# Optimization experiments

Hardware: AMD Instinct MI355X
Metric: run time of the kernel (lower is better)

The kernel has to match this reference:

```python
import jax, jax.numpy as jnp
import numpy as np

B, N, DIM = 2, 2048, 1024
HEADS, DIM_HEAD = 16, 64
ALIBI_HEADS = 8
NUM_MEM_KV = 4
SCALE = DIM_HEAD ** -0.5


def alibi_slopes(n):
    # standard ALiBi geometric slopes for power-of-2 head counts
    start = 2.0 ** (-8.0 / n)
    return jnp.array([start ** (k + 1) for k in range(n)], dtype=jnp.float32)


def alibi_bias(i, j, heads, total_heads):
    # symmetric ALiBi: bias = -|k_pos - q_pos| * slope; unbiased heads padded with zeros at front
    range_q = jnp.arange(j - i, j)          # query absolute positions (offset by mem kv)
    range_k = jnp.arange(j)
    rel = -jnp.abs(range_k[None, :] - range_q[:, None]).astype(jnp.float32)  # [i, j]
    slopes = alibi_slopes(heads)
    bias = slopes[:, None, None] * rel[None]                                  # [heads, i, j]
    pad = jnp.zeros((total_heads - heads, i, j), dtype=bias.dtype)
    return jnp.concatenate([pad, bias], axis=0)                               # [total_heads, i, j]


def setup_inputs() -> dict:
    key = jax.random.key(0)
    ks = jax.random.split(key, 7)
    w = lambda k, s: jax.random.normal(k, s, jnp.float32) * 0.02
    return {
        "x": jax.random.normal(ks[0], (B, N, DIM), jnp.float32),
        "mask": jnp.ones((B, N), dtype=bool),
        "Wq": w(ks[1], (DIM, HEADS * DIM_HEAD)),
        "Wk": w(ks[2], (DIM, HEADS * DIM_HEAD)),
        "Wv": w(ks[3], (DIM, HEADS * DIM_HEAD)),
        "Wo": w(ks[4], (HEADS * DIM_HEAD, DIM)),
        "mem_k": jax.random.normal(ks[5], (HEADS, NUM_MEM_KV, DIM_HEAD), jnp.float32),
        "mem_v": jax.random.normal(ks[6], (HEADS, NUM_MEM_KV, DIM_HEAD), jnp.float32),
    }


def reference(x, mask, Wq, Wk, Wv, Wo, mem_k, mem_v):
    b, n, _ = x.shape
    h, d, m = HEADS, DIM_HEAD, NUM_MEM_KV
    # QKV projections (Linear, no bias)
    q = (x @ Wq).reshape(b, n, h, d).transpose(0, 2, 1, 3)  # [b,h,n,d]
    k = (x @ Wk).reshape(b, n, h, d).transpose(0, 2, 1, 3)
    v = (x @ Wv).reshape(b, n, h, d).transpose(0, 2, 1, 3)
    # prepend learned memory key/values
    k = jnp.concatenate([jnp.broadcast_to(mem_k[None], (b, h, m, d)), k], axis=2)
    v = jnp.concatenate([jnp.broadcast_to(mem_v[None], (b, h, m, d)), v], axis=2)
    i, j = n, n + m
    # input mask padded with True over memory positions
    input_mask = jnp.concatenate([jnp.ones((b, m), dtype=bool), mask], axis=1)  # [b,j]
    # causal mask: key kj attendable by query qi iff kj - (j - i) <= qi (mem keys always visible)
    qpos = jnp.arange(i)[:, None]
    kpos = jnp.arange(j)[None, :]
    causal_allow = (kpos - (j - i)) <= qpos                                      # [i,j]
    allow = input_mask[:, None, None, :] & causal_allow[None, None]              # [b,1,i,j]
    bias = alibi_bias(i, j, ALIBI_HEADS, h)                                      # [h,i,j]
    scores = jnp.einsum('bhid,bhjd->bhij', q, k) * SCALE + bias[None]
    scores = jnp.where(allow, scores, jnp.finfo(scores.dtype).min)
    attn = jax.nn.softmax(scores, axis=-1)
    out = jnp.einsum('bhij,bhjd->bhid', attn, v)
    out = out.transpose(0, 2, 1, 3).reshape(b, n, h * d) @ Wo
    return out * mask[..., None].astype(out.dtype)
```

## Files before the change

### kernel.cpp

```cpp
#include <hip/hip_runtime.h>

typedef __bf16 bf16x8 __attribute__((ext_vector_type(8)));
typedef float f32x4 __attribute__((ext_vector_type(4)));
typedef unsigned short us8 __attribute__((ext_vector_type(8)));
typedef unsigned short ushort_t;
typedef unsigned int uint_t;

constexpr int BATCH = 2;
constexpr int SEQ   = 2048;
constexpr int DIM   = 1024;
constexpr int HEADS = 16;
constexpr int DH    = 64;
constexpr int NKV   = 4;
constexpr int KROWS = 2080;
constexpr int KVSTR = 133120;
constexpr float QSCALE = 0.18033688011112042f;

__device__ inline ushort_t f2bf(float f) {
  uint_t u = __builtin_bit_cast(uint_t, f);
  u += 0x7FFFu + ((u >> 16) & 1u);
  return (ushort_t)(u >> 16);
}

__device__ inline uint_t cvtpk(float a, float b) {
  uint_t r;
  asm("v_cvt_pk_bf16_f32 %0, %1, %2" : "=v"(r) : "v"(a), "v"(b));
  return r;
}

__device__ inline float ex2(float x) { return __builtin_amdgcn_exp2f(x); }

__device__ inline bf16x8 mk8(uint_t a, uint_t b, uint_t c, uint_t d) {
  union { uint_t u[4]; bf16x8 v; } x;
  x.u[0] = a; x.u[1] = b; x.u[2] = c; x.u[3] = d;
  return x.v;
}

__device__ inline size_t swz(int row, int k) {
  return ((size_t)(row >> 7) << 17) +
         (size_t)(((k >> 3) << 7) + (row & 127)) * 8 + (k & 7);
}

__device__ inline int koff(int j, int d) {
  return ((j >> 4) << 10) + ((d >> 3) << 7) + ((j & 15) << 3) + (d & 7);
}
__device__ inline int voff(int j, int d) {
  int w = j & 31;
  int kap = ((w & 12) << 1) | (w & 3) | ((w >> 4) << 2);
  return ((j >> 5) << 11) + ((kap >> 3) << 9) + (d << 3) + (kap & 7);
}

__device__ inline void g2l16(const ushort_t* g, ushort_t* l) {
  __builtin_amdgcn_global_load_lds(
      (const __attribute__((address_space(1))) void*)g,
      (__attribute__((address_space(3))) void*)l, 16, 0, 0);
}

__global__ __launch_bounds__(256) void prep_kernel(
    const float* __restrict__ x,
    const float* __restrict__ W0, const float* __restrict__ W1,
    const float* __restrict__ W2, const float* __restrict__ W3,
    const float* __restrict__ memk, const float* __restrict__ memv,
    ushort_t* __restrict__ xb,
    ushort_t* __restrict__ T0, ushort_t* __restrict__ T1,
    ushort_t* __restrict__ T2, ushort_t* __restrict__ T3,
    ushort_t* __restrict__ Vt, ushort_t* __restrict__ Ka)
{
  __shared__ float tile[32][33];
  int bid = blockIdx.x, t = threadIdx.x;
  if (bid < 2048) {
    int idx = bid * 256 + t;
    const float4* s = (const float4*)x;
    float4 a = s[idx * 2], bq = s[idx * 2 + 1];
    us8 o;
    o[0] = f2bf(a.x);  o[1] = f2bf(a.y);  o[2] = f2bf(a.z);  o[3] = f2bf(a.w);
    o[4] = f2bf(bq.x); o[5] = f2bf(bq.y); o[6] = f2bf(bq.z); o[7] = f2bf(bq.w);
    int e = idx * 8, row = e >> 10, k = e & 1023;
    *(us8*)&xb[swz(row, k)] = o;
  } else if (bid < 6144) {
    int tb = bid - 2048, z = tb >> 10, r2 = tb & 1023;
    int bx = r2 & 31, by = r2 >> 5;
    const float* W = (z == 0) ? W0 : (z == 1) ? W1 : (z == 2) ? W2 : W3;
    ushort_t* T = (z == 0) ? T0 : (z == 1) ? T1 : (z == 2) ? T2 : T3;
    float sc = (z == 0) ? QSCALE : 1.0f;
    int tx = t & 31, ty = t >> 5;
    int kb = bx * 32, nb = by * 32;
    for (int y = ty; y < 32; y += 8)
      tile[y][tx] = W[(size_t)(kb + y) * 1024 + nb + tx];
    __syncthreads();
    for (int y = ty; y < 32; y += 8)
      T[swz(nb + y, kb + tx)] = f2bf(tile[tx][y] * sc);
  } else {
    int idx = (bid - 6144) * 256 + t;
    if (idx < 8192) {
      int j = idx & 3, d = (idx >> 2) & 63, h = (idx >> 8) & 15, b = idx >> 12;
      Vt[(size_t)(b * 16 + h) * KVSTR + voff(j, d)] =
          f2bf(memv[((size_t)h * NKV + j) * DH + d]);
    } else if (idx < 16384) {
      int k2 = idx - 8192;
      int d = k2 & 63, j = (k2 >> 6) & 3, h = (k2 >> 8) & 15, b = k2 >> 12;
      Ka[(size_t)(b * 16 + h) * KVSTR + koff(j, d)] =
          f2bf(memk[((size_t)h * NKV + j) * DH + d]);
    }
  }
}

__global__ __launch_bounds__(256, 6) void gemm_bt(
    const ushort_t* __restrict__ A,
    const ushort_t* __restrict__ Wt0, const ushort_t* __restrict__ Wt1,
    const ushort_t* __restrict__ Wt2,
    ushort_t* __restrict__ C0, ushort_t* __restrict__ Ka,
    ushort_t* __restrict__ Vt)
{
  __shared__ ushort_t As[8192];
  __shared__ ushort_t Bs[4096];
  int bid = blockIdx.x;
  int xcd = bid & 7, g = bid >> 3;
  int z = g >> 6, rem = g & 63;
  int my = (xcd >> 1) * 8 + (rem >> 3);
  int nx = (xcd & 1) * 8 + (rem & 7);
  const ushort_t* Wt = (z == 1) ? Wt1 : (z == 2) ? Wt2 : Wt0;
  int t = threadIdx.x;
  int lane = t & 63, wave = t >> 6;
  int col = lane & 15, quad = lane >> 4;
  int m0 = my * 128, n0 = nx * 64;
  int moff = wave * 32;
  int nhalf = nx & 1;

  const ushort_t* Abase = A  + ((size_t)(m0 >> 7) << 17);
  const ushort_t* Bbase = Wt + ((size_t)(nx >> 1) << 17);
  int so = wave * 2048 + lane * 8;

  f32x4 acc[2][4] = {};

  for (int k0 = 0; k0 < DIM; k0 += 64) {
    __syncthreads();
    const ushort_t* Ak = Abase + ((size_t)k0 << 7);
    const ushort_t* Bk = Bbase + ((size_t)k0 << 7);
#pragma unroll
    for (int c2 = 0; c2 < 4; c2++)
      g2l16(Ak + so + c2 * 512, &As[so + c2 * 512]);
#pragma unroll
    for (int c2 = 0; c2 < 2; c2++) {
      int ko = wave * 2 + c2;
      g2l16(Bk + ko * 1024 + nhalf * 512 + lane * 8, &Bs[ko * 512 + lane * 8]);
    }
    __syncthreads();
#pragma unroll
    for (int kc = 0; kc < 2; kc++) {
      bf16x8 af[2], bfr[4];
#pragma unroll
      for (int mi = 0; mi < 2; mi++)
        af[mi] = *(const bf16x8*)&As[(kc * 4 + quad) * 1024 + (moff + mi * 16 + col) * 8];
#pragma unroll
      for (int ni = 0; ni < 4; ni++)
        bfr[ni] = *(const bf16x8*)&Bs[(kc * 4 + quad) * 512 + (ni * 16 + col) * 8];
#pragma unroll
      for (int mi = 0; mi < 2; mi++)
#pragma unroll
        for (int ni = 0; ni < 4; ni++)
          acc[mi][ni] = __builtin_amdgcn_mfma_f32_16x16x32_bf16(
              af[mi], bfr[ni], acc[mi][ni], 0, 0, 0);
    }
  }

  if (z == 0) {
#pragma unroll
    for (int mi = 0; mi < 2; mi++) {
      int row0 = m0 + moff + mi * 16 + quad * 4;
#pragma unroll
      for (int ni = 0; ni < 4; ni++) {
        int cn = n0 + ni * 16 + col;
#pragma unroll
        for (int r = 0; r < 4; r++)
          C0[swz(row0 + r, cn)] = f2bf(acc[mi][ni][r]);
      }
    }
  } else if (z == 1) {
#pragma unroll
    for (int mi = 0; mi < 2; mi++) {
      int gi = m0 + moff + mi * 16 + quad * 4;
      int bq = gi >> 11, i = gi & 2047;
#pragma unroll
      for (int ni = 0; ni < 4; ni++) {
        int feat = n0 + ni * 16 + col;
        int hh = feat >> 6, dd = feat & 63;
        size_t base = (size_t)(bq * 16 + hh) * KVSTR;
#pragma unroll
        for (int r = 0; r < 4; r++)
          Ka[base + koff(i + r + NKV, dd)] = f2bf(acc[mi][ni][r]);
      }
    }
  } else {
#pragma unroll
    for (int mi = 0; mi < 2; mi++) {
      int gi = m0 + moff + mi * 16 + quad * 4;
      int bq = gi >> 11, i = gi & 2047;
#pragma unroll
      for (int ni = 0; ni < 4; ni++) {
        int feat = n0 + ni * 16 + col;
        int hh = feat >> 6, dd = feat & 63;
        size_t vb = (size_t)(bq * 16 + hh) * KVSTR;
#pragma unroll
        for (int r = 0; r < 4; r++)
          Vt[vb + voff(i + r + NKV, dd)] = f2bf(acc[mi][ni][r]);
      }
    }
  }
}

__global__ __launch_bounds__(256, 4) void gemm_out64(
    const ushort_t* __restrict__ A, const ushort_t* __restrict__ Wt,
    float* __restrict__ Cf)
{
  __shared__ ushort_t As[4096];
  __shared__ ushort_t Bs[4096];
  int bid = blockIdx.x;
  int xcd = bid & 7, g = bid >> 3;
  int my = xcd * 8 + (g >> 4);
  int nx = g & 15;
  int t = threadIdx.x;
  int lane = t & 63, wave = t >> 6;
  int col = lane & 15, quad = lane >> 4;
  int m0 = my * 64, n0 = nx * 64;
  int mhalf = my & 1;
  int nhalf = nx & 1;

  const ushort_t* Abase = A  + ((size_t)(my >> 1) << 17);
  const ushort_t* Bbase = Wt + ((size_t)(nx >> 1) << 17);

  f32x4 acc[4] = {};

  for (int k0 = 0; k0 < DIM; k0 += 64) {
    __syncthreads();
    const ushort_t* Ak = Abase + ((size_t)k0 << 7);
    const ushort_t* Bk = Bbase + ((size_t)k0 << 7);
#pragma unroll
    for (int c2 = 0; c2 < 2; c2++) {
      int ko = wave * 2 + c2;
      g2l16(Ak + ko * 1024 + mhalf * 512 + lane * 8, &As[ko * 512 + lane * 8]);
      g2l16(Bk + ko * 1024 + nhalf * 512 + lane * 8, &Bs[ko * 512 + lane * 8]);
    }
    __syncthreads();
#pragma unroll
    for (int kc = 0; kc < 2; kc++) {
      bf16x8 af, bfr[4];
      af = *(const bf16x8*)&As[(kc * 4 + quad) * 512 + (wave * 16 + col) * 8];
#pragma unroll
      for (int ni = 0; ni < 4; ni++)
        bfr[ni] = *(const bf16x8*)&Bs[(kc * 4 + quad) * 512 + (ni * 16 + col) * 8];
#pragma unroll
      for (int ni = 0; ni < 4; ni++)
        acc[ni] = __builtin_amdgcn_mfma_f32_16x16x32_bf16(
            af, bfr[ni], acc[ni], 0, 0, 0);
    }
  }

  int row0 = m0 + wave * 16 + quad * 4;
#pragma unroll
  for (int ni = 0; ni < 4; ni++) {
    int cn = n0 + ni * 16 + col;
#pragma unroll
    for (int r = 0; r < 4; r++)
      Cf[(size_t)(row0 + r) * DIM + cn] = acc[ni][r];
  }
}

#define SUBITER(jbX, jpref, K0, K1, K2, K3, V0, V1, V2, V3)                   \
  {                                                                           \
    f32x4 s0a = {}, s1a = {}, s0b = {}, s1b = {};                             \
    __builtin_amdgcn_s_setprio(1);                                            \
    s0a = __builtin_amdgcn_mfma_f32_16x16x32_bf16(K0, qa0, s0a, 0, 0, 0);     \
    s0a = __builtin_amdgcn_mfma_f32_16x16x32_bf16(K1, qa1, s0a, 0, 0, 0);     \
    s1a = __builtin_amdgcn_mfma_f32_16x16x32_bf16(K2, qa0, s1a, 0, 0, 0);     \
    s1a = __builtin_amdgcn_mfma_f32_16x16x32_bf16(K3, qa1, s1a, 0, 0, 0);     \
    s0b = __builtin_amdgcn_mfma_f32_16x16x32_bf16(K0, qb0, s0b, 0, 0, 0);     \
    s0b = __builtin_amdgcn_mfma_f32_16x16x32_bf16(K1, qb1, s0b, 0, 0, 0);     \
    s1b = __builtin_amdgcn_mfma_f32_16x16x32_bf16(K2, qb0, s1b, 0, 0, 0);     \
    s1b = __builtin_amdgcn_mfma_f32_16x16x32_bf16(K3, qb1, s1b, 0, 0, 0);     \
    __builtin_amdgcn_s_setprio(0);                                            \
    int jc = (jpref) > 2048 ? 2048 : (jpref);                                 \
    int aK = jc * 64 + kOff;                                                  \
    K0 = *(const bf16x8*)&Kbh[aK];                                            \
    K1 = *(const bf16x8*)&Kbh[aK + 512];                                      \
    K2 = *(const bf16x8*)&Kbh[aK + 1024];                                     \
    K3 = *(const bf16x8*)&Kbh[aK + 1536];                                     \
    float fD0 = (float)((jbX) + quad * 4 - i0 - col - NKV);                   \
    bf16x8 pa, pb;                                                            \
    {                                                                         \
      f32x4 e0, e1;                                                           \
      if ((jbX) <= i0 - 27) {                                                 \
        _Pragma("unroll")                                                     \
        for (int r = 0; r < 4; r++) {                                         \
          e0[r] = ex2(fmaf(slope2, fD0 + (float)r, s0a[r]));                  \
          e1[r] = ex2(fmaf(slope2, fD0 + 16.0f + (float)r, s1a[r]));          \
        }                                                                     \
      } else {                                                                \
        _Pragma("unroll")                                                     \
        for (int r = 0; r < 4; r++) {                                         \
          float f0 = fD0 + (float)r, f1 = fD0 + 16.0f + (float)r;             \
          float w0 = fmaf(slope2, f0, s0a[r]);                                \
          float w1 = fmaf(slope2, f1, s1a[r]);                                \
          w0 = (f0 <= 0.0f) ? w0 : -1e30f;                                    \
          w1 = (f1 <= 0.0f) ? w1 : -1e30f;                                    \
          e0[r] = ex2(w0); e1[r] = ex2(w1);                                   \
        }                                                                     \
      }                                                                       \
      pa = mk8(cvtpk(e0[0], e0[1]), cvtpk(e0[2], e0[3]),                      \
               cvtpk(e1[0], e1[1]), cvtpk(e1[2], e1[3]));                     \
    }                                                                         \
    {                                                                         \
      float fDb = fD0 - 16.0f;                                                \
      f32x4 e0, e1;                                                           \
      if ((jbX) <= i0 - 11) {                                                 \
        _Pragma("unroll")                                                     \
        for (int r = 0; r < 4; r++) {                                         \
          e0[r] = ex2(fmaf(slope2, fDb + (float)r, s0b[r]));                  \
          e1[r] = ex2(fmaf(slope2, fDb + 16.0f + (float)r, s1b[r]));          \
        }                                                                     \
      } else {                                                                \
        _Pragma("unroll")                                                     \
        for (int r = 0; r < 4; r++) {                                         \
          float f0 = fDb + (float)r, f1 = fDb + 16.0f + (float)r;             \
          float w0 = fmaf(slope2, f0, s0b[r]);                                \
          float w1 = fmaf(slope2, f1, s1b[r]);                                \
          w0 = (f0 <= 0.0f) ? w0 : -1e30f;                                    \
          w1 = (f1 <= 0.0f) ? w1 : -1e30f;                                    \
          e0[r] = ex2(w0); e1[r] = ex2(w1);                                   \
        }                                                                     \
      }                                                                       \
      pb = mk8(cvtpk(e0[0], e0[1]), cvtpk(e0[2], e0[3]),                      \
               cvtpk(e1[0], e1[1]), cvtpk(e1[2], e1[3]));                     \
    }                                                                         \
    __builtin_amdgcn_s_setprio(1);                                            \
    o0a = __builtin_amdgcn_mfma_f32_16x16x32_bf16(pa, V0, o0a, 0, 0, 0);      \
    o1a = __builtin_amdgcn_mfma_f32_16x16x32_bf16(pa, V1, o1a, 0, 0, 0);      \
    o2a = __builtin_amdgcn_mfma_f32_16x16x32_bf16(pa, V2, o2a, 0, 0, 0);      \
    o3a = __builtin_amdgcn_mfma_f32_16x16x32_bf16(pa, V3, o3a, 0, 0, 0);      \
    ola = __builtin_amdgcn_mfma_f32_16x16x32_bf16(pa, ones, ola, 0, 0, 0);    \
    o0b = __builtin_amdgcn_mfma_f32_16x16x32_bf16(pb, V0, o0b, 0, 0, 0);      \
    o1b = __builtin_amdgcn_mfma_f32_16x16x32_bf16(pb, V1, o1b, 0, 0, 0);      \
    o2b = __builtin_amdgcn_mfma_f32_16x16x32_bf16(pb, V2, o2b, 0, 0, 0);      \
    o3b = __builtin_amdgcn_mfma_f32_16x16x32_bf16(pb, V3, o3b, 0, 0, 0);      \
    olb = __builtin_amdgcn_mfma_f32_16x16x32_bf16(pb, ones, olb, 0, 0, 0);    \
    __builtin_amdgcn_s_setprio(0);                                            \
    int aV = jc * 64 + vOff;                                                  \
    V0 = *(const bf16x8*)&Vbh[aV];                                            \
    V1 = *(const bf16x8*)&Vbh[aV + 128];                                      \
    V2 = *(const bf16x8*)&Vbh[aV + 256];                                      \
    V3 = *(const bf16x8*)&Vbh[aV + 384];                                      \
  }

__global__ __launch_bounds__(256) void attn_kernel(
    const ushort_t* __restrict__ Q, const ushort_t* __restrict__ Ka,
    const ushort_t* __restrict__ Vt, ushort_t* __restrict__ AO)
{
  __shared__ __align__(16) float Cmb[2][10][64][4];
  int t = threadIdx.x, lane = t & 63, wave = t >> 6;
  int col = lane & 15, quad = lane >> 4;
  int bid = blockIdx.x;
  int xcd = bid & 7, slot = bid >> 3;
  int bh = xcd + 8 * (slot >> 4);
  int b = bh >> 4, h = bh & 15;
  int u = slot & 15;
  int pi = u * 2 + (wave >> 1);
  int h2 = wave & 1;
  int p2 = wave >> 1;
  float slope2 = (h < 8) ? 0.0f : exp2f(-(float)(h - 7)) * 1.4426950408889634f;

  const ushort_t* Kbh = Ka + (size_t)bh * KVSTR;
  const ushort_t* Vbh = Vt + (size_t)bh * KVSTR;

  us8 ones_u = {0x3F80, 0x3F80, 0x3F80, 0x3F80, 0x3F80, 0x3F80, 0x3F80, 0x3F80};
  bf16x8 ones = __builtin_bit_cast(bf16x8, ones_u);

  int kOff = quad * 128 + col * 8;
  int vOff = quad * 512 + col * 8;

  for (int hv = 0; hv < 2; hv++) {
    int s = hv ? 63 - pi : pi;
    int i0 = s * 32;
    int jend = ((i0 + 67) >> 5) << 5;

    bf16x8 qa0 = *(const bf16x8*)&Q[swz(b * SEQ + i0 + col, h * DH + quad * 8)];
    bf16x8 qa1 = *(const bf16x8*)&Q[swz(b * SEQ + i0 + col, h * DH + 32 + quad * 8)];
    bf16x8 qb0 = *(const bf16x8*)&Q[swz(b * SEQ + i0 + 16 + col, h * DH + quad * 8)];
    bf16x8 qb1 = *(const bf16x8*)&Q[swz(b * SEQ + i0 + 16 + col, h * DH + 32 + quad * 8)];

    f32x4 o0a = {}, o1a = {}, o2a = {}, o3a = {}, ola = {};
    f32x4 o0b = {}, o1b = {}, o2b = {}, o3b = {}, olb = {};

    bf16x8 ka0, ka1, ka2, ka3, va0, va1, va2, va3;
    bf16x8 kb0, kb1, kb2, kb3, vb0, vb1, vb2, vb3;
    int jb0 = h2 * 32;
    {
      int aK = jb0 * 64 + kOff, aV = jb0 * 64 + vOff;
      ka0 = *(const bf16x8*)&Kbh[aK];
      ka1 = *(const bf16x8*)&Kbh[aK + 512];
      ka2 = *(const bf16x8*)&Kbh[aK + 1024];
      ka3 = *(const bf16x8*)&Kbh[aK + 1536];
      va0 = *(const bf16x8*)&Vbh[aV];
      va1 = *(const bf16x8*)&Vbh[aV + 128];
      va2 = *(const bf16x8*)&Vbh[aV + 256];
      va3 = *(const bf16x8*)&Vbh[aV + 384];
      int j1 = jb0 + 64;
      int bK = j1 * 64 + kOff, bV = j1 * 64 + vOff;
      kb0 = *(const bf16x8*)&Kbh[bK];
      kb1 = *(const bf16x8*)&Kbh[bK + 512];
      kb2 = *(const bf16x8*)&Kbh[bK + 1024];
      kb3 = *(const bf16x8*)&Kbh[bK + 1536];
      vb0 = *(const bf16x8*)&Vbh[bV];
      vb1 = *(const bf16x8*)&Vbh[bV + 128];
      vb2 = *(const bf16x8*)&Vbh[bV + 256];
      vb3 = *(const bf16x8*)&Vbh[bV + 384];
    }

    int ntrip = (jend - jb0 + 127) >> 7;
    int jb = jb0;
#pragma unroll 1
    for (int tr = 0; tr < ntrip; tr++, jb += 128) {
      SUBITER(jb, jb + 128, ka0, ka1, ka2, ka3, va0, va1, va2, va3);
      SUBITER(jb + 64, jb + 192, kb0, kb1, kb2, kb3, vb0, vb1, vb2, vb3);
    }

    if (h2 == 1) {
      *(f32x4*)&Cmb[p2][0][lane][0] = o0a;
      *(f32x4*)&Cmb[p2][1][lane][0] = o1a;
      *(f32x4*)&Cmb[p2][2][lane][0] = o2a;
      *(f32x4*)&Cmb[p2][3][lane][0] = o3a;
      *(f32x4*)&Cmb[p2][4][lane][0] = ola;
      *(f32x4*)&Cmb[p2][5][lane][0] = o0b;
      *(f32x4*)&Cmb[p2][6][lane][0] = o1b;
      *(f32x4*)&Cmb[p2][7][lane][0] = o2b;
      *(f32x4*)&Cmb[p2][8][lane][0] = o3b;
      *(f32x4*)&Cmb[p2][9][lane][0] = olb;
    }
    __syncthreads();
    if (h2 == 0) {
      o0a += *(const f32x4*)&Cmb[p2][0][lane][0];
      o1a += *(const f32x4*)&Cmb[p2][1][lane][0];
      o2a += *(const f32x4*)&Cmb[p2][2][lane][0];
      o3a += *(const f32x4*)&Cmb[p2][3][lane][0];
      ola += *(const f32x4*)&Cmb[p2][4][lane][0];
      o0b += *(const f32x4*)&Cmb[p2][5][lane][0];
      o1b += *(const f32x4*)&Cmb[p2][6][lane][0];
      o2b += *(const f32x4*)&Cmb[p2][7][lane][0];
      o3b += *(const f32x4*)&Cmb[p2][8][lane][0];
      olb += *(const f32x4*)&Cmb[p2][9][lane][0];
#pragma unroll
      for (int r = 0; r < 4; r++) {
        float linv = __builtin_amdgcn_rcpf(ola[r]);
        int row = b * SEQ + i0 + quad * 4 + r;
        AO[swz(row, h * DH + col)]      = f2bf(o0a[r] * linv);
        AO[swz(row, h * DH + 16 + col)] = f2bf(o1a[r] * linv);
        AO[swz(row, h * DH + 32 + col)] = f2bf(o2a[r] * linv);
        AO[swz(row, h * DH + 48 + col)] = f2bf(o3a[r] * linv);
      }
#pragma unroll
      for (int r = 0; r < 4; r++) {
        float linv = __builtin_amdgcn_rcpf(olb[r]);
        int row = b * SEQ + i0 + 16 + quad * 4 + r;
        AO[swz(row, h * DH + col)]      = f2bf(o0b[r] * linv);
        AO[swz(row, h * DH + 16 + col)] = f2bf(o1b[r] * linv);
        AO[swz(row, h * DH + 32 + col)] = f2bf(o2b[r] * linv);
        AO[swz(row, h * DH + 48 + col)] = f2bf(o3b[r] * linv);
      }
    }
    __syncthreads();
  }
}
#undef SUBITER

extern "C" void kernel_launch(void* const* d_in, const int* in_sizes, int n_in,
                              void* d_out, int out_size, void* d_ws, size_t ws_size,
                              hipStream_t stream)
{
  const float* x    = (const float*)d_in[0];
  const float* Wq   = (const float*)d_in[2];
  const float* Wk   = (const float*)d_in[3];
  const float* Wv   = (const float*)d_in[4];
  const float* Wo   = (const float*)d_in[5];
  const float* memk = (const float*)d_in[6];
  const float* memv = (const float*)d_in[7];
  float* out = (float*)d_out;

  char* ws = (char*)d_ws;
  size_t off = 0;
  auto alloc = [&](size_t bytes) {
    char* p = ws + off;
    off += (bytes + 255) & ~(size_t)255;
    return p;
  };
  ushort_t* WqT = (ushort_t*)alloc((size_t)1024 * 1024 * 2);
  ushort_t* WkT = (ushort_t*)alloc((size_t)1024 * 1024 * 2);
  ushort_t* WvT = (ushort_t*)alloc((size_t)1024 * 1024 * 2);
  ushort_t* WoT = (ushort_t*)alloc((size_t)1024 * 1024 * 2);
  ushort_t* xb  = (ushort_t*)alloc((size_t)4096 * 1024 * 2);
  ushort_t* Qb  = (ushort_t*)alloc((size_t)4096 * 1024 * 2);
  ushort_t* Ka  = (ushort_t*)alloc((size_t)32 * KVSTR * 2);
  ushort_t* Vt  = (ushort_t*)alloc((size_t)32 * KVSTR * 2);
  ushort_t* AO  = xb;

  prep_kernel<<<dim3(6208), dim3(256), 0, stream>>>(
      x, Wq, Wk, Wv, Wo, memk, memv, xb, WqT, WkT, WvT, WoT, Vt, Ka);
  gemm_bt<<<dim3(1536), dim3(256), 0, stream>>>(xb, WqT, WkT, WvT, Qb, Ka, Vt);
  attn_kernel<<<dim3(512), dim3(256), 0, stream>>>(Qb, Ka, Vt, AO);
  gemm_out64<<<dim3(1024), dim3(256), 0, stream>>>(AO, WoT, out);
}
```

Measured before the change: 169.0 us.

## Fuse Q/K/V projection GEMMs into one block sharing the A tile

Each block now computes the Q, K and V output tiles for the same 128x64 region, loading the x tile once and three weight tiles per k-step. This replaces three separate blocks per tile, cutting redundant A-tile global loads and LDS fills to a third. Blocks grow to 512 threads with each wave owning 16 rows across three accumulators, so the grid shrinks from 1536 to 512 blocks. That may reduce occupancy and latency hiding, and it raises LDS use per block.

```diff
diff --git a/kernel.cpp b/kernel.cpp
--- a/kernel.cpp
+++ b/kernel.cpp
@@ -105,7 +105,7 @@
   }
 }
 
-__global__ __launch_bounds__(256, 6) void gemm_bt(
+__global__ __launch_bounds__(512) void gemm_bt(
     const ushort_t* __restrict__ A,
     const ushort_t* __restrict__ Wt0, const ushort_t* __restrict__ Wt1,
     const ushort_t* __restrict__ Wt2,
@@ -113,98 +113,87 @@
     ushort_t* __restrict__ Vt)
 {
   __shared__ ushort_t As[8192];
-  __shared__ ushort_t Bs[4096];
+  __shared__ ushort_t Bs[12288];
   int bid = blockIdx.x;
   int xcd = bid & 7, g = bid >> 3;
-  int z = g >> 6, rem = g & 63;
-  int my = (xcd >> 1) * 8 + (rem >> 3);
-  int nx = (xcd & 1) * 8 + (rem & 7);
-  const ushort_t* Wt = (z == 1) ? Wt1 : (z == 2) ? Wt2 : Wt0;
+  int my = (xcd >> 1) * 8 + (g >> 3);
+  int nx = (xcd & 1) * 8 + (g & 7);
   int t = threadIdx.x;
   int lane = t & 63, wave = t >> 6;
   int col = lane & 15, quad = lane >> 4;
   int m0 = my * 128, n0 = nx * 64;
-  int moff = wave * 32;
+  int moff = wave * 16;
   int nhalf = nx & 1;
 
-  const ushort_t* Abase = A  + ((size_t)(m0 >> 7) << 17);
-  const ushort_t* Bbase = Wt + ((size_t)(nx >> 1) << 17);
-  int so = wave * 2048 + lane * 8;
-
-  f32x4 acc[2][4] = {};
+  const ushort_t* Abase = A + ((size_t)(m0 >> 7) << 17);
+  size_t boff = (size_t)(nx >> 1) << 17;
+  const ushort_t* Bb0 = Wt0 + boff;
+  const ushort_t* Bb1 = Wt1 + boff;
+  const ushort_t* Bb2 = Wt2 + boff;
+  int t8 = t * 8;
+  int bo = (t >> 6) * 1024 + nhalf * 512 + (t & 63) * 8;
+
+  f32x4 acc[3][4] = {};
 
   for (int k0 = 0; k0 < DIM; k0 += 64) {
     __syncthreads();
     const ushort_t* Ak = Abase + ((size_t)k0 << 7);
-    const ushort_t* Bk = Bbase + ((size_t)k0 << 7);
-#pragma unroll
-    for (int c2 = 0; c2 < 4; c2++)
-      g2l16(Ak + so + c2 * 512, &As[so + c2 * 512]);
-#pragma unroll
-    for (int c2 = 0; c2 < 2; c2++) {
-      int ko = wave * 2 + c2;
-      g2l16(Bk + ko * 1024 + nhalf * 512 + lane * 8, &Bs[ko * 512 + lane * 8]);
-    }
+    size_t ko2 = (size_t)k0 << 7;
+    g2l16(Ak + t8, &As[t8]);
+    g2l16(Ak + t8 + 4096, &As[t8 + 4096]);
+    g2l16(Bb0 + ko2 + bo, &Bs[t8]);
+    g2l16(Bb1 + ko2 + bo, &Bs[4096 + t8]);
+    g2l16(Bb2 + ko2 + bo, &Bs[8192 + t8]);
     __syncthreads();
 #pragma unroll
     for (int kc = 0; kc < 2; kc++) {
-      bf16x8 af[2], bfr[4];
-#pragma unroll
-      for (int mi = 0; mi < 2; mi++)
-        af[mi] = *(const bf16x8*)&As[(kc * 4 + quad) * 1024 + (moff + mi * 16 + col) * 8];
-#pragma unroll
-      for (int ni = 0; ni < 4; ni++)
-        bfr[ni] = *(const bf16x8*)&Bs[(kc * 4 + quad) * 512 + (ni * 16 + col) * 8];
-#pragma unroll
-      for (int mi = 0; mi < 2; mi++)
+      bf16x8 af = *(const bf16x8*)&As[(kc * 4 + quad) * 1024 + (moff + col) * 8];
+#pragma unroll
+      for (int z = 0; z < 3; z++) {
+        bf16x8 bfr[4];
 #pragma unroll
         for (int ni = 0; ni < 4; ni++)
-          acc[mi][ni] = __builtin_amdgcn_mfma_f32_16x16x32_bf16(
-              af[mi], bfr[ni], acc[mi][ni], 0, 0, 0);
-    }
-  }
-
-  if (z == 0) {
-#pragma unroll
-    for (int mi = 0; mi < 2; mi++) {
-      int row0 = m0 + moff + mi * 16 + quad * 4;
-#pragma unroll
-      for (int ni = 0; ni < 4; ni++) {
-        int cn = n0 + ni * 16 + col;
-#pragma unroll
-        for (int r = 0; r < 4; r++)
-          C0[swz(row0 + r, cn)] = f2bf(acc[mi][ni][r]);
+          bfr[ni] = *(const bf16x8*)&Bs[z * 4096 + (kc * 4 + quad) * 512 + (ni * 16 + col) * 8];
+#pragma unroll
+        for (int ni = 0; ni < 4; ni++)
+          acc[z][ni] = __builtin_amdgcn_mfma_f32_16x16x32_bf16(
+              af, bfr[ni], acc[z][ni], 0, 0, 0);
       }
     }
-  } else if (z == 1) {
-#pragma unroll
-    for (int mi = 0; mi < 2; mi++) {
-      int gi = m0 + moff + mi * 16 + quad * 4;
-      int bq = gi >> 11, i = gi & 2047;
-#pragma unroll
-      for (int ni = 0; ni < 4; ni++) {
-        int feat = n0 + ni * 16 + col;
-        int hh = feat >> 6, dd = feat & 63;
-        size_t base = (size_t)(bq * 16 + hh) * KVSTR;
-#pragma unroll
-        for (int r = 0; r < 4; r++)
-          Ka[base + koff(i + r + NKV, dd)] = f2bf(acc[mi][ni][r]);
-      }
-    }
-  } else {
-#pragma unroll
-    for (int mi = 0; mi < 2; mi++) {
-      int gi = m0 + moff + mi * 16 + quad * 4;
-      int bq = gi >> 11, i = gi & 2047;
-#pragma unroll
-      for (int ni = 0; ni < 4; ni++) {
-        int feat = n0 + ni * 16 + col;
-        int hh = feat >> 6, dd = feat & 63;
-        size_t vb = (size_t)(bq * 16 + hh) * KVSTR;
-#pragma unroll
-        for (int r = 0; r < 4; r++)
-          Vt[vb + voff(i + r + NKV, dd)] = f2bf(acc[mi][ni][r]);
-      }
+  }
+
+  int row0 = m0 + moff + quad * 4;
+  {
+#pragma unroll
+    for (int ni = 0; ni < 4; ni++) {
+      int cn = n0 + ni * 16 + col;
+#pragma unroll
+      for (int r = 0; r < 4; r++)
+        C0[swz(row0 + r, cn)] = f2bf(acc[0][ni][r]);
+    }
+  }
+  {
+    int bq = row0 >> 11, i = row0 & 2047;
+#pragma unroll
+    for (int ni = 0; ni < 4; ni++) {
+      int feat = n0 + ni * 16 + col;
+      int hh = feat >> 6, dd = feat & 63;
+      size_t base = (size_t)(bq * 16 + hh) * KVSTR;
+#pragma unroll
+      for (int r = 0; r < 4; r++)
+        Ka[base + koff(i + r + NKV, dd)] = f2bf(acc[1][ni][r]);
+    }
+  }
+  {
+    int bq = row0 >> 11, i = row0 & 2047;
+#pragma unroll
+    for (int ni = 0; ni < 4; ni++) {
+      int feat = n0 + ni * 16 + col;
+      int hh = feat >> 6, dd = feat & 63;
+      size_t vb = (size_t)(bq * 16 + hh) * KVSTR;
+#pragma unroll
+      for (int r = 0; r < 4; r++)
+        Vt[vb + voff(i + r + NKV, dd)] = f2bf(acc[2][ni][r]);
     }
   }
 }
@@ -503,7 +492,7 @@
 
   prep_kernel<<<dim3(6208), dim3(256), 0, stream>>>(
       x, Wq, Wk, Wv, Wo, memk, memv, xb, WqT, WkT, WvT, WoT, Vt, Ka);
-  gemm_bt<<<dim3(1536), dim3(256), 0, stream>>>(xb, WqT, WkT, WvT, Qb, Ka, Vt);
+  gemm_bt<<<dim3(512), dim3(512), 0, stream>>>(xb, WqT, WkT, WvT, Qb, Ka, Vt);
   attn_kernel<<<dim3(512), dim3(256), 0, stream>>>(Qb, Ka, Vt, AO);
   gemm_out64<<<dim3(1024), dim3(256), 0, stream>>>(AO, WoT, out);
 }
```

After: 173.0 us. +2.3%, slower.
